# Kernel optimization log

Measured on AMD Instinct MI355X. Metric: run time of the kernel, lower is better.

The kernel has to match this reference:

```python
import jax, jax.numpy as jnp
import numpy as np

L, D, H, KS, VS, HID = 2048, 1024, 16, 1024, 1024, 4096
EPS = 1e-5


def _linear_params(key, din, dout):
    # torch nn.Linear default init: U(-1/sqrt(din), 1/sqrt(din))
    s = 1.0 / np.sqrt(din)
    kw, kb = jax.random.split(key)
    W = jax.random.uniform(kw, (dout, din), minval=-s, maxval=s, dtype=jnp.float32)
    b = jax.random.uniform(kb, (dout,), minval=-s, maxval=s, dtype=jnp.float32)
    return W, b


def setup_inputs() -> dict:
    key = jax.random.key(0)
    ks = jax.random.split(key, 12)
    x = jax.random.normal(ks[0], (L, D), dtype=jnp.float32)
    # inverse shortest-path lengths in [0, 1]
    shortest_path = jax.random.uniform(ks[1], (L, L), dtype=jnp.float32)
    Wq, bq = _linear_params(ks[2], D, KS)
    Wk, bk = _linear_params(ks[3], D, KS)
    Wv, bv = _linear_params(ks[4], D, VS)
    Wqp, bqp = _linear_params(ks[5], KS, KS)
    Wkp, bkp = _linear_params(ks[6], KS, KS)
    Wvp, bvp = _linear_params(ks[7], VS, VS)
    Wo, bo = _linear_params(ks[8], VS, D)
    W1, b1 = _linear_params(ks[9], D, HID)
    W2, b2 = _linear_params(ks[10], HID, D)
    g1 = jnp.ones((D,), jnp.float32); be1 = jnp.zeros((D,), jnp.float32)
    g2 = jnp.ones((D,), jnp.float32); be2 = jnp.zeros((D,), jnp.float32)
    return dict(x=x, shortest_path=shortest_path,
                Wq=Wq, bq=bq, Wk=Wk, bk=bk, Wv=Wv, bv=bv,
                Wqp=Wqp, bqp=bqp, Wkp=Wkp, bkp=bkp, Wvp=Wvp, bvp=bvp,
                Wo=Wo, bo=bo, W1=W1, b1=b1, W2=W2, b2=b2,
                g1=g1, be1=be1, g2=g2, be2=be2)


def _dense(h, W, b):
    return h @ W.T + b


def _layernorm(h, g, b):
    mu = jnp.mean(h, axis=-1, keepdims=True)
    var = jnp.mean(jnp.square(h - mu), axis=-1, keepdims=True)
    return (h - mu) * jax.lax.rsqrt(var + EPS) * g + b


def reference(x, shortest_path, Wq, bq, Wk, bk, Wv, bv, Wqp, bqp, Wkp, bkp,
              Wvp, bvp, Wo, bo, W1, b1, W2, b2, g1, be1, g2, be2):
    hd = KS // H
    vhd = VS // H
    q = _dense(_dense(x, Wq, bq), Wqp, bqp).reshape(L, H, hd).transpose(1, 0, 2)   # [H,L,hd]
    k = _dense(_dense(x, Wk, bk), Wkp, bkp).reshape(L, H, hd).transpose(1, 0, 2)   # [H,L,hd]
    v = _dense(_dense(x, Wv, bv), Wvp, bvp).reshape(L, H, vhd).transpose(1, 0, 2)  # [H,L,vhd]
    att = jnp.einsum('hld,hmd->hlm', q, k) / jnp.sqrt(jnp.float32(hd))             # [H,L,L]
    sp_bias = jax.nn.softmax(shortest_path, axis=-1) * 0.5                          # [L,L]
    att = jax.nn.softmax(att + sp_bias[None, :, :], axis=-1)
    o = jnp.einsum('hlm,hmd->hld', att, v).transpose(1, 0, 2).reshape(L, VS)        # [L,VS]
    o = _dense(o, Wo, bo)
    h = _layernorm(x + o, g1, be1)                # residual + LN1 (dropout=identity)
    f = jax.nn.relu(_dense(jax.nn.relu(_dense(h, W1, b1)), W2, b2))
    return _layernorm(h + f, g2, be2)             # residual + LN2
```

## Files before the change

### kernel.cpp

```cpp
#include <hip/hip_runtime.h>

typedef __attribute__((ext_vector_type(4))) float f32x4;
typedef __attribute__((ext_vector_type(8))) short s16x8;

static __device__ __forceinline__ ushort f2b(float f) {
  union { float f; unsigned u; } v; v.f = f;
  unsigned u = v.u;
  unsigned r = (u + 0x7fffu + ((u >> 16) & 1u)) >> 16;
  return (ushort)r;
}
static __device__ __forceinline__ float b2f(ushort h) {
  union { unsigned u; float f; } v; v.u = ((unsigned)h) << 16;
  return v.f;
}
static __device__ __forceinline__ unsigned cvtpk(float a, float b) {
  unsigned r;
  asm("v_cvt_pk_bf16_f32 %0, %1, %2" : "=v"(r) : "v"(a), "v"(b));
  return r;
}
static __device__ __forceinline__ float exp2i(float x) {
  float r;
  asm("v_exp_f32 %0, %1" : "=v"(r) : "v"(x));
  return r;
}

static __device__ __forceinline__ void gload_lds16(const ushort* g, ushort* l) {
  __builtin_amdgcn_global_load_lds(
      (const __attribute__((address_space(1))) void*)g,
      (__attribute__((address_space(3))) void*)l, 16, 0, 0);
}

#define LOG2E 1.44269504f

struct Cvt7 {
  const float* src[7];
  ushort* dst[7];
  int n[7];
};
__global__ __launch_bounds__(256) void cvt_multi_k(Cvt7 a) {
  int e = blockIdx.y;
  int i = (blockIdx.x * 256 + threadIdx.x) * 4;
  if (i >= a.n[e]) return;
  float4 v4 = *(const float4*)(a.src[e] + i);
  ushort4 o4; o4.x = f2b(v4.x); o4.y = f2b(v4.y); o4.z = f2b(v4.z); o4.w = f2b(v4.w);
  *(ushort4*)(a.dst[e] + i) = o4;
}

__global__ __launch_bounds__(256) void wtr_k(const float* __restrict__ Wq,
                                             const float* __restrict__ Wk,
                                             const float* __restrict__ Wv,
                                             ushort* __restrict__ dst) {
  __shared__ float t[64][65];
  int z = blockIdx.z;
  const float* src = z == 0 ? Wq : (z == 1 ? Wk : Wv);
  float scale = z == 0 ? 0.125f * LOG2E : 1.f;
  int r0 = blockIdx.x * 64, c0 = blockIdx.y * 64;
  int lr = threadIdx.x >> 2, lc4 = (threadIdx.x & 3) * 16;
#pragma unroll
  for (int j = 0; j < 4; ++j)
    *(float4*)&t[lr][lc4 + j * 4] = *(const float4*)(src + (size_t)(r0 + lr) * 1024 + c0 + lc4 + j * 4);
  __syncthreads();
  ushort tmp[16];
#pragma unroll
  for (int j = 0; j < 16; ++j) tmp[j] = f2b(t[lc4 + j][lr] * scale);
  ushort* d = dst + (size_t)z * 1048576 + (size_t)(c0 + lr) * 1024 + r0 + lc4;
  *(uint4*)d = *(uint4*)tmp;
  *(uint4*)(d + 8) = *(uint4*)(tmp + 8);
}

__global__ __launch_bounds__(256) void bvec_k(
    const float* __restrict__ Wqp, const float* __restrict__ Wkp, const float* __restrict__ Wvp,
    const float* __restrict__ bq, const float* __restrict__ bqp,
    const float* __restrict__ bk, const float* __restrict__ bkp,
    const float* __restrict__ bv, const float* __restrict__ bvp,
    float* __restrict__ outb) {
  int r = blockIdx.x * 4 + (threadIdx.x >> 6);
  int lane = threadIdx.x & 63;
  int z = r >> 10, rr = r & 1023;
  const float* Wp = z == 0 ? Wqp : (z == 1 ? Wkp : Wvp);
  const float* bi = z == 0 ? bq : (z == 1 ? bk : bv);
  const float* bp = z == 0 ? bqp : (z == 1 ? bkp : bvp);
  float s = 0.f;
#pragma unroll
  for (int t = 0; t < 4; ++t) {
    float4 w = *(const float4*)(Wp + (size_t)rr * 1024 + lane * 16 + t * 4);
    float4 b = *(const float4*)(bi + lane * 16 + t * 4);
    s += w.x * b.x + w.y * b.y + w.z * b.z + w.w * b.w;
  }
#pragma unroll
  for (int m = 1; m < 64; m <<= 1) s += __shfl_xor(s, m);
  if (lane == 0) outb[r] = (s + bp[rr]) * (z == 0 ? 0.125f * LOG2E : 1.f);
}

__global__ __launch_bounds__(256) void spsm_k(const float* __restrict__ sp,
                                              ushort* __restrict__ outP) {
  const int Lc = 2048;
  int row = blockIdx.x;
  int tid = threadIdx.x;
  const float* r = sp + (size_t)row * Lc;
  float v[8];
  float mx = -1e30f;
#pragma unroll
  for (int j = 0; j < 8; ++j) { v[j] = r[tid + j * 256]; mx = fmaxf(mx, v[j]); }
#pragma unroll
  for (int m = 1; m < 64; m <<= 1) mx = fmaxf(mx, __shfl_xor(mx, m));
  __shared__ float redm[4], reds[4];
  if ((tid & 63) == 0) redm[tid >> 6] = mx;
  __syncthreads();
  mx = fmaxf(fmaxf(redm[0], redm[1]), fmaxf(redm[2], redm[3]));
  float s = 0.f;
#pragma unroll
  for (int j = 0; j < 8; ++j) { v[j] = __expf(v[j] - mx); s += v[j]; }
#pragma unroll
  for (int m = 1; m < 64; m <<= 1) s += __shfl_xor(s, m);
  if ((tid & 63) == 0) reds[tid >> 6] = s;
  __syncthreads();
  s = reds[0] + reds[1] + reds[2] + reds[3];
  float inv = 0.5f * LOG2E / s;
  int mb = row >> 6, rr = row & 63;
  int wv = rr >> 4, rem = rr & 15, rg = rem >> 2, ii = rem & 3;
  size_t rbase = ((size_t)mb * 32) * 4096 + (size_t)wv * 1024 + (size_t)ii * 256 + (size_t)rg * 16;
#pragma unroll
  for (int j = 0; j < 8; ++j) {
    int col = tid + j * 256;
    int nb = col >> 6, cc = col & 63, nt = cc >> 4, cl = cc & 15;
    outP[rbase + (size_t)nb * 4096 + nt * 64 + cl] = f2b(v[j] * inv);
  }
}

__global__ __launch_bounds__(256) void vtr_k(const ushort* __restrict__ qkv,
                                             ushort* __restrict__ vT) {
  __shared__ ushort t[64][72];
  int tid = threadIdx.x;
  int r = tid >> 3, c8 = (tid & 7) * 8;
  int l0 = blockIdx.x * 64, h = blockIdx.y;
#pragma unroll
  for (int p = 0; p < 2; ++p)
    *(uint4*)&t[r + p * 32][c8] =
        *(const uint4*)(qkv + (size_t)(l0 + r + p * 32) * 3072 + 2048 + h * 64 + c8);
  __syncthreads();
#pragma unroll
  for (int p = 0; p < 2; ++p) {
    int d = r + p * 32;
    ushort tmp[8];
#pragma unroll
    for (int j = 0; j < 8; ++j) tmp[j] = t[c8 + j][d];
    *(uint4*)(vT + ((size_t)h * 64 + d) * 2048 + l0 + c8) = *(uint4*)tmp;
  }
}

template <int BM, int ZM>
__global__ __launch_bounds__(256, BM == 64 ? 3 : 2) void gemm_k(
    const ushort* __restrict__ A, const ushort* __restrict__ W,
    const float* __restrict__ bias, void* __restrict__ Cv,
    int M, int N, int K, int relu, float oscale) {
  constexpr int MT = BM / 32;
  __shared__ ushort As0[BM][64], Bs0[128][64];
  __shared__ ushort As1[BM][64], Bs1[128][64];
  const int z = (ZM != 0) ? blockIdx.z : 0;
  if (ZM == 1) { A += (size_t)z * M * K; W += (size_t)z * N * K; }
  int kb0 = 0, kb1 = K;
  if (ZM == 2) { int kh = K >> 1; kb0 = z * kh; kb1 = kb0 + kh; }
  const int tid = threadIdx.x;
  const int lane = tid & 63;
  const int wave = tid >> 6;
  const int wm = (wave >> 1) * (BM / 2);
  const int wn = (wave & 1) * 64;
  const int bm = blockIdx.x * BM;
  const int bn = blockIdx.y * 128;
  const int cl = lane & 15, rg = lane >> 4;
  const int lrow = lane >> 3, lcol = (lane & 7) * 8;

  f32x4 acc[MT][4];
#pragma unroll
  for (int i = 0; i < MT; ++i)
#pragma unroll
    for (int j = 0; j < 4; ++j) acc[i][j] = (f32x4){0.f, 0.f, 0.f, 0.f};

  const ushort* gA = A + (size_t)(bm + wave * 8 + lrow) * K + lcol;
  const ushort* gB = W + (size_t)(bn + wave * 8 + lrow) * K + lcol;

  auto stage = [&](ushort* lA, ushort* lB, int k0) {
#pragma unroll
    for (int c = 0; c < MT; ++c)
      gload_lds16(gA + (size_t)(c * 32) * K + k0, lA + wave * 512 + c * 2048);
#pragma unroll
    for (int c = 0; c < 4; ++c)
      gload_lds16(gB + (size_t)(c * 32) * K + k0, lB + wave * 512 + c * 2048);
  };
  auto compute = [&](const ushort* As, const ushort* Bs) {
    const int kbo = 8 * rg;
#pragma unroll
    for (int kk = 0; kk < 64; kk += 32) {
      s16x8 af[MT], bf[4];
#pragma unroll
      for (int mt = 0; mt < MT; ++mt)
        af[mt] = *(const s16x8*)(As + (wm + mt * 16 + cl) * 64 + kk + kbo);
#pragma unroll
      for (int nt = 0; nt < 4; ++nt)
        bf[nt] = *(const s16x8*)(Bs + (wn + nt * 16 + cl) * 64 + kk + kbo);
#pragma unroll
      for (int mt = 0; mt < MT; ++mt)
#pragma unroll
        for (int nt = 0; nt < 4; ++nt)
          acc[mt][nt] = __builtin_amdgcn_mfma_f32_16x16x32_bf16(af[mt], bf[nt], acc[mt][nt], 0, 0, 0);
    }
  };

  const int ktiles = (kb1 - kb0) >> 6;
  stage(&As0[0][0], &Bs0[0][0], kb0);
  __syncthreads();
  for (int tt = 0; tt < ktiles; tt += 2) {
    stage(&As1[0][0], &Bs1[0][0], kb0 + (tt + 1) * 64);
    compute(&As0[0][0], &Bs0[0][0]);
    __syncthreads();
    if (tt + 2 < ktiles) stage(&As0[0][0], &Bs0[0][0], kb0 + (tt + 2) * 64);
    compute(&As1[0][0], &Bs1[0][0]);
    __syncthreads();
  }

  if (ZM == 2) {
    float* Cf = (float*)Cv + (size_t)z * M * N;
#pragma unroll
    for (int nt = 0; nt < 4; ++nt) {
      int c = bn + wn + nt * 16 + cl;
#pragma unroll
      for (int mt = 0; mt < MT; ++mt)
#pragma unroll
        for (int i = 0; i < 4; ++i) {
          int r = bm + wm + mt * 16 + rg * 4 + i;
          Cf[(size_t)r * N + c] = acc[mt][nt][i];
        }
    }
  } else {
    ushort* Cu = (ushort*)Cv;
    if (ZM == 1) Cu += (size_t)z * M * N;
#pragma unroll
    for (int nt = 0; nt < 4; ++nt) {
      int c = bn + wn + nt * 16 + cl;
      float bv = bias ? bias[c] : 0.f;
#pragma unroll
      for (int mt = 0; mt < MT; ++mt) {
        float v0 = (acc[mt][nt][0] + bv) * oscale;
        float v1 = (acc[mt][nt][1] + bv) * oscale;
        float v2 = (acc[mt][nt][2] + bv) * oscale;
        float v3 = (acc[mt][nt][3] + bv) * oscale;
        if (relu) {
          v0 = fmaxf(v0, 0.f); v1 = fmaxf(v1, 0.f);
          v2 = fmaxf(v2, 0.f); v3 = fmaxf(v3, 0.f);
        }
        unsigned p01 = cvtpk(v0, v1), p23 = cvtpk(v2, v3);
        size_t b = (size_t)(bm + wm + mt * 16 + rg * 4) * N + c;
        Cu[b] = (ushort)p01;
        Cu[b + N] = (ushort)(p01 >> 16);
        Cu[b + 2 * N] = (ushort)p23;
        Cu[b + 3 * N] = (ushort)(p23 >> 16);
      }
    }
  }
}

__global__ __launch_bounds__(256, 4) void attn_k(
    const ushort* __restrict__ qkv, const ushort* __restrict__ vT,
    const ushort* __restrict__ biasP, ushort* __restrict__ opart,
    float* __restrict__ lbuf) {
  const int Lc = 2048;
  int h = blockIdx.x;
  int m0 = blockIdx.y * 64;
  int s = blockIdx.z;
  int nb = s * 1024, ne = nb + 1024;
  int tid = threadIdx.x, lane = tid & 63, wave = tid >> 6;

  __shared__ ushort Ks[64][72];
  __shared__ ushort Vs[64][72];
  __shared__ ushort Ps[4][16][72];

  const int rg = lane >> 4, cl = lane & 15;
  const int kb = 8 * rg;
  int srow = tid >> 3, scol = (tid & 7) * 8;

  const ushort* qp = qkv + (size_t)(m0 + wave * 16 + cl) * 3072 + h * 64;
  s16x8 qfr0 = *(const s16x8*)(qp + kb);
  s16x8 qfr1 = *(const s16x8*)(qp + 32 + kb);

  const ushort* bpB = biasP + ((size_t)(m0 >> 6) * 32) * 4096 + (size_t)wave * 1024 + lane;

  f32x4 oacc[4];
#pragma unroll
  for (int i = 0; i < 4; ++i) oacc[i] = (f32x4){0.f, 0.f, 0.f, 0.f};
  float lacc[4] = {0.f, 0.f, 0.f, 0.f};

  for (int n0 = nb; n0 < ne; n0 += 64) {
    __syncthreads();
#pragma unroll
    for (int pp = 0; pp < 2; ++pp) {
      int r = srow + pp * 32;
      *(uint4*)&Ks[r][scol] = *(const uint4*)(qkv + (size_t)(n0 + r) * 3072 + 1024 + h * 64 + scol);
      *(uint4*)&Vs[r][scol] = *(const uint4*)(vT + ((size_t)h * 64 + r) * 2048 + n0 + scol);
    }
    __syncthreads();

    const ushort* bp = bpB + (size_t)(n0 >> 6) * 4096;
    f32x4 sacc[4];
#pragma unroll
    for (int i = 0; i < 4; ++i)
#pragma unroll
      for (int nt = 0; nt < 4; ++nt)
        sacc[nt][i] = b2f(bp[(i * 4 + nt) * 64]) - 8.f * LOG2E;

    __builtin_amdgcn_s_setprio(1);
#pragma unroll
    for (int nt = 0; nt < 4; ++nt) {
      s16x8 b = *(const s16x8*)&Ks[nt * 16 + cl][kb];
      sacc[nt] = __builtin_amdgcn_mfma_f32_16x16x32_bf16(qfr0, b, sacc[nt], 0, 0, 0);
    }
#pragma unroll
    for (int nt = 0; nt < 4; ++nt) {
      s16x8 b = *(const s16x8*)&Ks[nt * 16 + cl][32 + kb];
      sacc[nt] = __builtin_amdgcn_mfma_f32_16x16x32_bf16(qfr1, b, sacc[nt], 0, 0, 0);
    }
    __builtin_amdgcn_s_setprio(0);

#pragma unroll
    for (int i = 0; i < 4; ++i) {
#pragma unroll
      for (int nt = 0; nt < 4; ++nt) {
        float pv = exp2i(sacc[nt][i]);
        sacc[nt][i] = pv;
        lacc[i] += pv;
      }
    }
#pragma unroll
    for (int nt = 0; nt < 4; ++nt) {
      unsigned p01 = cvtpk(sacc[nt][0], sacc[nt][1]);
      unsigned p23 = cvtpk(sacc[nt][2], sacc[nt][3]);
      Ps[wave][rg * 4 + 0][nt * 16 + cl] = (ushort)p01;
      Ps[wave][rg * 4 + 1][nt * 16 + cl] = (ushort)(p01 >> 16);
      Ps[wave][rg * 4 + 2][nt * 16 + cl] = (ushort)p23;
      Ps[wave][rg * 4 + 3][nt * 16 + cl] = (ushort)(p23 >> 16);
    }
    __builtin_amdgcn_s_setprio(1);
#pragma unroll
    for (int kk = 0; kk < 64; kk += 32) {
      s16x8 a = *(const s16x8*)&Ps[wave][cl][kk + kb];
#pragma unroll
      for (int nt = 0; nt < 4; ++nt) {
        s16x8 b = *(const s16x8*)&Vs[nt * 16 + cl][kk + kb];
        oacc[nt] = __builtin_amdgcn_mfma_f32_16x16x32_bf16(a, b, oacc[nt], 0, 0, 0);
      }
    }
    __builtin_amdgcn_s_setprio(0);
  }
#pragma unroll
  for (int nt = 0; nt < 4; ++nt) {
    unsigned p01 = cvtpk(oacc[nt][0], oacc[nt][1]);
    unsigned p23 = cvtpk(oacc[nt][2], oacc[nt][3]);
    size_t b = ((size_t)s * Lc + (m0 + wave * 16 + rg * 4)) * 1024 + h * 64 + nt * 16 + cl;
    opart[b] = (ushort)p01;
    opart[b + 1024] = (ushort)(p01 >> 16);
    opart[b + 2048] = (ushort)p23;
    opart[b + 3072] = (ushort)(p23 >> 16);
  }
#pragma unroll
  for (int i = 0; i < 4; ++i) {
    float l = lacc[i];
#pragma unroll
    for (int m = 1; m < 16; m <<= 1) l += __shfl_xor(l, m);
    if (cl == 0) {
      int r = m0 + wave * 16 + rg * 4 + i;
      lbuf[(size_t)(s * 16 + h) * Lc + r] = l;
    }
  }
}

__global__ __launch_bounds__(256) void acomb_k(const ushort* __restrict__ op,
                                               const float* __restrict__ lbuf,
                                               ushort* __restrict__ ob) {
  const int Lc = 2048;
  int qrow = blockIdx.x;
  int tid = threadIdx.x;
  int c = tid * 4;
  int h = c >> 6;
  float l0 = lbuf[(size_t)h * Lc + qrow];
  float l1 = lbuf[(size_t)(16 + h) * Lc + qrow];
  float inv = 1.f / (l0 + l1);
  ushort4 a = *(const ushort4*)(op + (size_t)qrow * 1024 + c);
  ushort4 b = *(const ushort4*)(op + ((size_t)Lc + qrow) * 1024 + c);
  ushort4 o;
  o.x = f2b((b2f(a.x) + b2f(b.x)) * inv);
  o.y = f2b((b2f(a.y) + b2f(b.y)) * inv);
  o.z = f2b((b2f(a.z) + b2f(b.z)) * inv);
  o.w = f2b((b2f(a.w) + b2f(b.w)) * inv);
  *(ushort4*)(ob + (size_t)qrow * 1024 + c) = o;
}

__global__ __launch_bounds__(256) void lnf_k(const float* __restrict__ basef,
                                             const float* __restrict__ p,
                                             const float* __restrict__ bvec,
                                             const float* __restrict__ g,
                                             const float* __restrict__ be,
                                             int relu,
                                             ushort* __restrict__ outb,
                                             float* __restrict__ outf) {
  const int Dc = 1024;
  const size_t MN = (size_t)2048 * 1024;
  int row = blockIdx.x;
  int tid = threadIdx.x;
  int c = tid * 4;
  float4 bx = *(const float4*)(basef + (size_t)row * Dc + c);
  float4 a0 = *(const float4*)(p + (size_t)row * Dc + c);
  float4 a1 = *(const float4*)(p + MN + (size_t)row * Dc + c);
  float4 bb = *(const float4*)(bvec + c);
  float v0 = a0.x + a1.x + bb.x, v1 = a0.y + a1.y + bb.y;
  float v2 = a0.z + a1.z + bb.z, v3 = a0.w + a1.w + bb.w;
  if (relu) {
    v0 = fmaxf(v0, 0.f); v1 = fmaxf(v1, 0.f);
    v2 = fmaxf(v2, 0.f); v3 = fmaxf(v3, 0.f);
  }
  v0 += bx.x; v1 += bx.y; v2 += bx.z; v3 += bx.w;
  float s = v0 + v1 + v2 + v3;
  __shared__ float red[4];
#pragma unroll
  for (int m = 1; m < 64; m <<= 1) s += __shfl_xor(s, m);
  if ((tid & 63) == 0) red[tid >> 6] = s;
  __syncthreads();
  s = red[0] + red[1] + red[2] + red[3];
  float mu = s * (1.f / Dc);
  float d0 = v0 - mu, d1 = v1 - mu, d2 = v2 - mu, d3 = v3 - mu;
  float ss = d0 * d0 + d1 * d1 + d2 * d2 + d3 * d3;
  __syncthreads();
#pragma unroll
  for (int m = 1; m < 64; m <<= 1) ss += __shfl_xor(ss, m);
  if ((tid & 63) == 0) red[tid >> 6] = ss;
  __syncthreads();
  ss = red[0] + red[1] + red[2] + red[3];
  float rs = rsqrtf(ss * (1.f / Dc) + 1e-5f);
  float4 gv = *(const float4*)(g + c);
  float4 bev = *(const float4*)(be + c);
  float y0 = d0 * rs * gv.x + bev.x;
  float y1 = d1 * rs * gv.y + bev.y;
  float y2 = d2 * rs * gv.z + bev.z;
  float y3 = d3 * rs * gv.w + bev.w;
  size_t o = (size_t)row * Dc + c;
  if (outb) {
    ushort4 ob4; ob4.x = f2b(y0); ob4.y = f2b(y1); ob4.z = f2b(y2); ob4.w = f2b(y3);
    *(ushort4*)(outb + o) = ob4;
  }
  if (outf) {
    float4 of4; of4.x = y0; of4.y = y1; of4.z = y2; of4.w = y3;
    *(float4*)(outf + o) = of4;
  }
}

extern "C" void kernel_launch(void* const* d_in, const int* in_sizes, int n_in,
                              void* d_out, int out_size, void* d_ws, size_t ws_size,
                              hipStream_t stream) {
  const int L = 2048, D = 1024, H = 16, HID = 4096;
  const float* x   = (const float*)d_in[0];
  const float* sp  = (const float*)d_in[1];
  const float* Wq  = (const float*)d_in[2];  const float* bq  = (const float*)d_in[3];
  const float* Wk  = (const float*)d_in[4];  const float* bk  = (const float*)d_in[5];
  const float* Wv  = (const float*)d_in[6];  const float* bv  = (const float*)d_in[7];
  const float* Wqp = (const float*)d_in[8];  const float* bqp = (const float*)d_in[9];
  const float* Wkp = (const float*)d_in[10]; const float* bkp = (const float*)d_in[11];
  const float* Wvp = (const float*)d_in[12]; const float* bvp = (const float*)d_in[13];
  const float* Wo  = (const float*)d_in[14]; const float* bo  = (const float*)d_in[15];
  const float* W1  = (const float*)d_in[16]; const float* b1  = (const float*)d_in[17];
  const float* W2  = (const float*)d_in[18]; const float* b2  = (const float*)d_in[19];
  const float* g1  = (const float*)d_in[20]; const float* be1 = (const float*)d_in[21];
  const float* g2  = (const float*)d_in[22]; const float* be2 = (const float*)d_in[23];
  float* out = (float*)d_out;

  size_t off = 0;
  char* base = (char*)d_ws;
  auto alloc = [&](size_t b) {
    char* p = base + off;
    off += (b + 255) & ~(size_t)255;
    return p;
  };
  ushort* xb    = (ushort*)alloc((size_t)L * D * 2);
  ushort* wqpb  = (ushort*)alloc((size_t)D * D * 2);
  ushort* wkpb  = (ushort*)alloc((size_t)D * D * 2);
  ushort* wvpb  = (ushort*)alloc((size_t)D * D * 2);
  ushort* wqTb  = (ushort*)alloc((size_t)3 * D * D * 2);
  ushort* wfused= (ushort*)alloc((size_t)3 * D * D * 2);
  ushort* qkv   = (ushort*)alloc((size_t)L * 3072 * 2);
  float*  bfused= (float*)alloc((size_t)3072 * 4);
  ushort* wob   = (ushort*)alloc((size_t)D * D * 2);
  ushort* w1b   = (ushort*)alloc((size_t)HID * D * 2);
  ushort* w2b   = (ushort*)alloc((size_t)D * HID * 2);
  ushort* spsb  = (ushort*)alloc((size_t)L * L * 2);
  ushort* opart = (ushort*)alloc((size_t)2 * L * 1024 * 2);
  ushort* vT    = (ushort*)alloc((size_t)H * 64 * L * 2);
  float*  lbuf  = (float*)alloc((size_t)2 * H * L * 4);
  ushort* ob    = (ushort*)alloc((size_t)L * 1024 * 2);
  ushort* hb    = (ushort*)alloc((size_t)L * D * 2);
  float*  hf    = (float*)alloc((size_t)L * D * 4);

  ushort* ffn1  = wqTb;
  float*  parts = (float*)spsb;

  Cvt7 ca;
  ca.src[0] = x;   ca.dst[0] = xb;   ca.n[0] = L * D;
  ca.src[1] = Wqp; ca.dst[1] = wqpb; ca.n[1] = D * D;
  ca.src[2] = Wkp; ca.dst[2] = wkpb; ca.n[2] = D * D;
  ca.src[3] = Wvp; ca.dst[3] = wvpb; ca.n[3] = D * D;
  ca.src[4] = Wo;  ca.dst[4] = wob;  ca.n[4] = D * D;
  ca.src[5] = W1;  ca.dst[5] = w1b;  ca.n[5] = HID * D;
  ca.src[6] = W2;  ca.dst[6] = w2b;  ca.n[6] = D * HID;
  cvt_multi_k<<<dim3(4096, 7), dim3(256), 0, stream>>>(ca);

  wtr_k<<<dim3(16, 16, 3), dim3(256), 0, stream>>>(Wq, Wk, Wv, wqTb);
  bvec_k<<<dim3(768), dim3(256), 0, stream>>>(Wqp, Wkp, Wvp, bq, bqp, bk, bkp, bv, bvp, bfused);
  spsm_k<<<dim3(L), dim3(256), 0, stream>>>(sp, spsb);

  gemm_k<64, 1><<<dim3(16, 8, 3), dim3(256), 0, stream>>>(
      wqpb, wqTb, (const float*)nullptr, wfused, D, D, D, 0, 1.f);
  gemm_k<64, 0><<<dim3(32, 24), dim3(256), 0, stream>>>(
      xb, wfused, bfused, qkv, L, 3072, D, 0, 1.f);

  vtr_k<<<dim3(L / 64, H), dim3(256), 0, stream>>>(qkv, vT);
  attn_k<<<dim3(H, L / 64, 2), dim3(256), 0, stream>>>(qkv, vT, spsb, opart, lbuf);
  acomb_k<<<dim3(L), dim3(256), 0, stream>>>(opart, lbuf, ob);

  gemm_k<64, 2><<<dim3(32, 8, 2), dim3(256), 0, stream>>>(
      ob, wob, (const float*)nullptr, parts, L, D, D, 0, 1.f);
  lnf_k<<<dim3(L), dim3(256), 0, stream>>>(x, parts, bo, g1, be1, 0, hb, hf);
  gemm_k<128, 0><<<dim3(16, 32), dim3(256), 0, stream>>>(
      hb, w1b, b1, ffn1, L, HID, D, 1, 1.f);
  gemm_k<64, 2><<<dim3(32, 8, 2), dim3(256), 0, stream>>>(
      ffn1, w2b, (const float*)nullptr, parts, L, D, HID, 0, 1.f);
  lnf_k<<<dim3(L), dim3(256), 0, stream>>>(hf, parts, b2, g2, be2, 1, (ushort*)nullptr, out);
}
```

Measured before the change: 215.7 us.

## Double attention query tile per block and split keys into four chunks

Each attention block now handles 128 query rows as two 64-row halves that share every K/V tile staged in LDS. This halves global K/V loads per unit of work, and the key range is split four ways instead of two so the grid size stays the same. The combine kernel now sums four partial outputs and row sums, which doubles the partial-output traffic and doubles the accumulator registers per thread. The constant offset subtracted before exp2 is also dropped, since it cancels in the normalisation. Without it, large scores have less headroom against overflow.

```diff
diff --git a/kernel.cpp b/kernel.cpp
--- a/kernel.cpp
+++ b/kernel.cpp
@@ -266,29 +266,36 @@
     float* __restrict__ lbuf) {
   const int Lc = 2048;
   int h = blockIdx.x;
-  int m0 = blockIdx.y * 64;
+  int m0 = blockIdx.y * 128;
   int s = blockIdx.z;
-  int nb = s * 1024, ne = nb + 1024;
+  int nb = s * 512, ne = nb + 512;
   int tid = threadIdx.x, lane = tid & 63, wave = tid >> 6;
 
   __shared__ ushort Ks[64][72];
   __shared__ ushort Vs[64][72];
-  __shared__ ushort Ps[4][16][72];
+  __shared__ ushort Ps[4][2][16][72];
 
   const int rg = lane >> 4, cl = lane & 15;
   const int kb = 8 * rg;
   int srow = tid >> 3, scol = (tid & 7) * 8;
 
-  const ushort* qp = qkv + (size_t)(m0 + wave * 16 + cl) * 3072 + h * 64;
-  s16x8 qfr0 = *(const s16x8*)(qp + kb);
-  s16x8 qfr1 = *(const s16x8*)(qp + 32 + kb);
-
-  const ushort* bpB = biasP + ((size_t)(m0 >> 6) * 32) * 4096 + (size_t)wave * 1024 + lane;
-
-  f32x4 oacc[4];
-#pragma unroll
-  for (int i = 0; i < 4; ++i) oacc[i] = (f32x4){0.f, 0.f, 0.f, 0.f};
-  float lacc[4] = {0.f, 0.f, 0.f, 0.f};
+  s16x8 qfr[2][2];
+#pragma unroll
+  for (int mh = 0; mh < 2; ++mh) {
+    const ushort* qp = qkv + (size_t)(m0 + mh * 64 + wave * 16 + cl) * 3072 + h * 64;
+    qfr[mh][0] = *(const s16x8*)(qp + kb);
+    qfr[mh][1] = *(const s16x8*)(qp + 32 + kb);
+  }
+
+  const ushort* bpB0 = biasP + ((size_t)(m0 >> 6) * 32) * 4096 + (size_t)wave * 1024 + lane;
+  const ushort* bpB1 = bpB0 + (size_t)32 * 4096;
+
+  f32x4 oacc[2][4];
+#pragma unroll
+  for (int mh = 0; mh < 2; ++mh)
+#pragma unroll
+    for (int i = 0; i < 4; ++i) oacc[mh][i] = (f32x4){0.f, 0.f, 0.f, 0.f};
+  float lacc[2][4] = {{0.f, 0.f, 0.f, 0.f}, {0.f, 0.f, 0.f, 0.f}};
 
   for (int n0 = nb; n0 < ne; n0 += 64) {
     __syncthreads();
@@ -300,75 +307,84 @@
     }
     __syncthreads();
 
-    const ushort* bp = bpB + (size_t)(n0 >> 6) * 4096;
-    f32x4 sacc[4];
-#pragma unroll
-    for (int i = 0; i < 4; ++i)
-#pragma unroll
-      for (int nt = 0; nt < 4; ++nt)
-        sacc[nt][i] = b2f(bp[(i * 4 + nt) * 64]) - 8.f * LOG2E;
+#pragma unroll
+    for (int mh = 0; mh < 2; ++mh) {
+      const ushort* bp = (mh ? bpB1 : bpB0) + (size_t)(n0 >> 6) * 4096;
+      f32x4 sacc[4];
+#pragma unroll
+      for (int i = 0; i < 4; ++i)
+#pragma unroll
+        for (int nt = 0; nt < 4; ++nt)
+          sacc[nt][i] = b2f(bp[(i * 4 + nt) * 64]);
+
+      __builtin_amdgcn_s_setprio(1);
+#pragma unroll
+      for (int kk2 = 0; kk2 < 2; ++kk2) {
+#pragma unroll
+        for (int nt = 0; nt < 4; ++nt) {
+          s16x8 b = *(const s16x8*)&Ks[nt * 16 + cl][kk2 * 32 + kb];
+          sacc[nt] = __builtin_amdgcn_mfma_f32_16x16x32_bf16(qfr[mh][kk2], b, sacc[nt], 0, 0, 0);
+        }
+      }
+      __builtin_amdgcn_s_setprio(0);
+
+#pragma unroll
+      for (int i = 0; i < 4; ++i) {
+#pragma unroll
+        for (int nt = 0; nt < 4; ++nt) {
+          float pv = exp2i(sacc[nt][i]);
+          sacc[nt][i] = pv;
+          lacc[mh][i] += pv;
+        }
+      }
+#pragma unroll
+      for (int nt = 0; nt < 4; ++nt) {
+        unsigned p01 = cvtpk(sacc[nt][0], sacc[nt][1]);
+        unsigned p23 = cvtpk(sacc[nt][2], sacc[nt][3]);
+        Ps[wave][mh][rg * 4 + 0][nt * 16 + cl] = (ushort)p01;
+        Ps[wave][mh][rg * 4 + 1][nt * 16 + cl] = (ushort)(p01 >> 16);
+        Ps[wave][mh][rg * 4 + 2][nt * 16 + cl] = (ushort)p23;
+        Ps[wave][mh][rg * 4 + 3][nt * 16 + cl] = (ushort)(p23 >> 16);
+      }
+    }
 
     __builtin_amdgcn_s_setprio(1);
 #pragma unroll
+    for (int mh = 0; mh < 2; ++mh) {
+#pragma unroll
+      for (int kk = 0; kk < 64; kk += 32) {
+        s16x8 a = *(const s16x8*)&Ps[wave][mh][cl][kk + kb];
+#pragma unroll
+        for (int nt = 0; nt < 4; ++nt) {
+          s16x8 b = *(const s16x8*)&Vs[nt * 16 + cl][kk + kb];
+          oacc[mh][nt] = __builtin_amdgcn_mfma_f32_16x16x32_bf16(a, b, oacc[mh][nt], 0, 0, 0);
+        }
+      }
+    }
+    __builtin_amdgcn_s_setprio(0);
+  }
+
+#pragma unroll
+  for (int mh = 0; mh < 2; ++mh) {
+#pragma unroll
     for (int nt = 0; nt < 4; ++nt) {
-      s16x8 b = *(const s16x8*)&Ks[nt * 16 + cl][kb];
-      sacc[nt] = __builtin_amdgcn_mfma_f32_16x16x32_bf16(qfr0, b, sacc[nt], 0, 0, 0);
-    }
-#pragma unroll
-    for (int nt = 0; nt < 4; ++nt) {
-      s16x8 b = *(const s16x8*)&Ks[nt * 16 + cl][32 + kb];
-      sacc[nt] = __builtin_amdgcn_mfma_f32_16x16x32_bf16(qfr1, b, sacc[nt], 0, 0, 0);
-    }
-    __builtin_amdgcn_s_setprio(0);
-
+      unsigned p01 = cvtpk(oacc[mh][nt][0], oacc[mh][nt][1]);
+      unsigned p23 = cvtpk(oacc[mh][nt][2], oacc[mh][nt][3]);
+      size_t b = ((size_t)s * Lc + (m0 + mh * 64 + wave * 16 + rg * 4)) * 1024 + h * 64 + nt * 16 + cl;
+      opart[b] = (ushort)p01;
+      opart[b + 1024] = (ushort)(p01 >> 16);
+      opart[b + 2048] = (ushort)p23;
+      opart[b + 3072] = (ushort)(p23 >> 16);
+    }
 #pragma unroll
     for (int i = 0; i < 4; ++i) {
-#pragma unroll
-      for (int nt = 0; nt < 4; ++nt) {
-        float pv = exp2i(sacc[nt][i]);
-        sacc[nt][i] = pv;
-        lacc[i] += pv;
+      float l = lacc[mh][i];
+#pragma unroll
+      for (int m = 1; m < 16; m <<= 1) l += __shfl_xor(l, m);
+      if (cl == 0) {
+        int r = m0 + mh * 64 + wave * 16 + rg * 4 + i;
+        lbuf[(size_t)(s * 16 + h) * Lc + r] = l;
       }
-    }
-#pragma unroll
-    for (int nt = 0; nt < 4; ++nt) {
-      unsigned p01 = cvtpk(sacc[nt][0], sacc[nt][1]);
-      unsigned p23 = cvtpk(sacc[nt][2], sacc[nt][3]);
-      Ps[wave][rg * 4 + 0][nt * 16 + cl] = (ushort)p01;
-      Ps[wave][rg * 4 + 1][nt * 16 + cl] = (ushort)(p01 >> 16);
-      Ps[wave][rg * 4 + 2][nt * 16 + cl] = (ushort)p23;
-      Ps[wave][rg * 4 + 3][nt * 16 + cl] = (ushort)(p23 >> 16);
-    }
-    __builtin_amdgcn_s_setprio(1);
-#pragma unroll
-    for (int kk = 0; kk < 64; kk += 32) {
-      s16x8 a = *(const s16x8*)&Ps[wave][cl][kk + kb];
-#pragma unroll
-      for (int nt = 0; nt < 4; ++nt) {
-        s16x8 b = *(const s16x8*)&Vs[nt * 16 + cl][kk + kb];
-        oacc[nt] = __builtin_amdgcn_mfma_f32_16x16x32_bf16(a, b, oacc[nt], 0, 0, 0);
-      }
-    }
-    __builtin_amdgcn_s_setprio(0);
-  }
-#pragma unroll
-  for (int nt = 0; nt < 4; ++nt) {
-    unsigned p01 = cvtpk(oacc[nt][0], oacc[nt][1]);
-    unsigned p23 = cvtpk(oacc[nt][2], oacc[nt][3]);
-    size_t b = ((size_t)s * Lc + (m0 + wave * 16 + rg * 4)) * 1024 + h * 64 + nt * 16 + cl;
-    opart[b] = (ushort)p01;
-    opart[b + 1024] = (ushort)(p01 >> 16);
-    opart[b + 2048] = (ushort)p23;
-    opart[b + 3072] = (ushort)(p23 >> 16);
-  }
-#pragma unroll
-  for (int i = 0; i < 4; ++i) {
-    float l = lacc[i];
-#pragma unroll
-    for (int m = 1; m < 16; m <<= 1) l += __shfl_xor(l, m);
-    if (cl == 0) {
-      int r = m0 + wave * 16 + rg * 4 + i;
-      lbuf[(size_t)(s * 16 + h) * Lc + r] = l;
     }
   }
 }
@@ -381,16 +397,19 @@
   int tid = threadIdx.x;
   int c = tid * 4;
   int h = c >> 6;
-  float l0 = lbuf[(size_t)h * Lc + qrow];
-  float l1 = lbuf[(size_t)(16 + h) * Lc + qrow];
-  float inv = 1.f / (l0 + l1);
-  ushort4 a = *(const ushort4*)(op + (size_t)qrow * 1024 + c);
-  ushort4 b = *(const ushort4*)(op + ((size_t)Lc + qrow) * 1024 + c);
+  float lsum = 0.f;
+#pragma unroll
+  for (int s = 0; s < 4; ++s) lsum += lbuf[(size_t)(s * 16 + h) * Lc + qrow];
+  float inv = 1.f / lsum;
+  float acc0 = 0.f, acc1 = 0.f, acc2 = 0.f, acc3 = 0.f;
+#pragma unroll
+  for (int s = 0; s < 4; ++s) {
+    ushort4 a = *(const ushort4*)(op + ((size_t)s * Lc + qrow) * 1024 + c);
+    acc0 += b2f(a.x); acc1 += b2f(a.y); acc2 += b2f(a.z); acc3 += b2f(a.w);
+  }
   ushort4 o;
-  o.x = f2b((b2f(a.x) + b2f(b.x)) * inv);
-  o.y = f2b((b2f(a.y) + b2f(b.y)) * inv);
-  o.z = f2b((b2f(a.z) + b2f(b.z)) * inv);
-  o.w = f2b((b2f(a.w) + b2f(b.w)) * inv);
+  o.x = f2b(acc0 * inv); o.y = f2b(acc1 * inv);
+  o.z = f2b(acc2 * inv); o.w = f2b(acc3 * inv);
   *(ushort4*)(ob + (size_t)qrow * 1024 + c) = o;
 }
 
@@ -490,9 +509,9 @@
   ushort* w1b   = (ushort*)alloc((size_t)HID * D * 2);
   ushort* w2b   = (ushort*)alloc((size_t)D * HID * 2);
   ushort* spsb  = (ushort*)alloc((size_t)L * L * 2);
-  ushort* opart = (ushort*)alloc((size_t)2 * L * 1024 * 2);
+  ushort* opart = (ushort*)alloc((size_t)4 * L * 1024 * 2);
   ushort* vT    = (ushort*)alloc((size_t)H * 64 * L * 2);
-  float*  lbuf  = (float*)alloc((size_t)2 * H * L * 4);
+  float*  lbuf  = (float*)alloc((size_t)4 * H * L * 4);
   ushort* ob    = (ushort*)alloc((size_t)L * 1024 * 2);
   ushort* hb    = (ushort*)alloc((size_t)L * D * 2);
   float*  hf    = (float*)alloc((size_t)L * D * 4);
@@ -520,7 +539,7 @@
       xb, wfused, bfused, qkv, L, 3072, D, 0, 1.f);
 
   vtr_k<<<dim3(L / 64, H), dim3(256), 0, stream>>>(qkv, vT);
-  attn_k<<<dim3(H, L / 64, 2), dim3(256), 0, stream>>>(qkv, vT, spsb, opart, lbuf);
+  attn_k<<<dim3(H, L / 128, 4), dim3(256), 0, stream>>>(qkv, vT, spsb, opart, lbuf);
   acomb_k<<<dim3(L), dim3(256), 0, stream>>>(opart, lbuf, ob);
 
   gemm_k<64, 2><<<dim3(32, 8, 2), dim3(256), 0, stream>>>(
```

New measurement: 212.6 us. Within noise of the previous version (-1.4%).
